# Kernel optimization log

Measured on AMD Instinct MI355X. Metric: run time of the kernel, lower is better.

Reference implementation:

```python
import jax, jax.numpy as jnp
import numpy as np

WINDOW = 64
STRIDE = 4
IMG_H = 512
IMG_W = 512


def _extract_windows(img, W, stride):
    # img: [H, Wd] -> windows [oh*ow, W, W] (row-major over the output grid,
    # matching torch F.unfold ordering)
    H, Wd = img.shape
    oh = (H - W) // stride + 1
    ow = (Wd - W) // stride + 1
    rows = (jnp.arange(oh) * stride)[:, None] + jnp.arange(W)[None, :]   # [oh, W]
    cols = (jnp.arange(ow) * stride)[:, None] + jnp.arange(W)[None, :]   # [ow, W]
    windows = img[rows[:, None, :, None], cols[None, :, None, :]]        # [oh, ow, W, W]
    return windows.reshape(oh * ow, W, W), oh, ow


def setup_inputs() -> dict:
    key = jax.random.key(0)
    X = jax.random.uniform(key, (1, 1, IMG_H, IMG_W), dtype=jnp.float32)
    return {"X": X}


def reference(X):
    W = WINDOW
    stride = STRIDE
    img = X[0, 0]
    windows, oh, ow = _extract_windows(img, W, stride)  # [N, W, W]

    # sizes = 2**arange(log2(W), 1, -1): e.g. W=64 -> [64, 32, 16, 8, 4]
    sizes = (2 ** np.arange(int(np.log2(W)), 1, -1)).astype(np.int64)
    log_sizes = jnp.log(jnp.asarray(sizes, dtype=jnp.float32))  # [S]

    log_db = []
    for s in sizes:
        s = int(s)
        # box partition of each window: [N, W//s, s, W//s, s]
        r = windows.reshape(-1, W // s, s, W // s, s)
        smax = r.max(axis=(2, 4))
        smin = r.min(axis=(2, 4))
        d_b = (smax - smin).sum(axis=(1, 2))  # [N] per-window box-count sum
        log_db.append(jnp.log(d_b))
    log_db = jnp.stack(log_db)  # [S, N]

    # lstsq with a single column (no intercept): slope = <x, y> / <x, x>
    slope = (log_sizes @ log_db) / (log_sizes @ log_sizes)  # [N]
    fd = -slope
    return fd.reshape(1, 1, oh, ow)
```

## Files before the change

### kernel.cpp

```cpp
#include <hip/hip_runtime.h>
#include <math.h>

#define IMG_W 512
#define OW 113
#define DS 27

__device__ __forceinline__ float max4f(float4 v) { return fmaxf(fmaxf(v.x, v.y), fmaxf(v.z, v.w)); }
__device__ __forceinline__ float min4f(float4 v) { return fminf(fminf(v.x, v.y), fminf(v.z, v.w)); }

__global__ __launch_bounds__(256) void fd_fused(const float* __restrict__ X,
                                                float* __restrict__ out) {
    const int bi = blockIdx.x / 15;
    const int bj = blockIdx.x - bi * 15;
    const int t  = threadIdx.x;

    __shared__ float tmax[23][24], tmin[23][24];
    __shared__ float p8x[22][24],  p8n[22][24];
    __shared__ float p16x[20][24], p16n[20][24];
    __shared__ float p32x[16][24], p32n[16][24];
    __shared__ float df4[23][DS], df8[22][DS], df16[20][DS], df32[16][DS];

    for (int idx = t; idx < 23 * 23; idx += 256) {
        const int lr = idx / 23, lc = idx - lr * 23;
        const int gr = min(bi * 8 + lr, 127);
        const int gc = min(bj * 8 + lc, 127);
        const float* p = X + (gr * 4) * IMG_W + gc * 4;
        float4 a = *(const float4*)(p);
        float4 b = *(const float4*)(p + IMG_W);
        float4 c = *(const float4*)(p + 2 * IMG_W);
        float4 d = *(const float4*)(p + 3 * IMG_W);
        float mx = fmaxf(fmaxf(max4f(a), max4f(b)), fmaxf(max4f(c), max4f(d)));
        float mn = fminf(fminf(min4f(a), min4f(b)), fminf(min4f(c), min4f(d)));
        tmax[lr][lc] = mx;
        tmin[lr][lc] = mn;
        df4[lr][lc]  = mx - mn;
    }
    __syncthreads();

    for (int idx = t; idx < 22 * 22; idx += 256) {
        const int lr = idx / 22, lc = idx - lr * 22;
        float x = fmaxf(fmaxf(tmax[lr][lc],     tmax[lr][lc + 1]),
                        fmaxf(tmax[lr + 1][lc], tmax[lr + 1][lc + 1]));
        float n = fminf(fminf(tmin[lr][lc],     tmin[lr][lc + 1]),
                        fminf(tmin[lr + 1][lc], tmin[lr + 1][lc + 1]));
        p8x[lr][lc] = x;
        p8n[lr][lc] = n;
        df8[lr][lc] = x - n;
    }
    __syncthreads();

    for (int idx = t; idx < 20 * 20; idx += 256) {
        const int lr = idx / 20, lc = idx - lr * 20;
        float x = fmaxf(fmaxf(p8x[lr][lc],     p8x[lr][lc + 2]),
                        fmaxf(p8x[lr + 2][lc], p8x[lr + 2][lc + 2]));
        float n = fminf(fminf(p8n[lr][lc],     p8n[lr][lc + 2]),
                        fminf(p8n[lr + 2][lc], p8n[lr + 2][lc + 2]));
        p16x[lr][lc] = x;
        p16n[lr][lc] = n;
        df16[lr][lc] = x - n;
    }
    __syncthreads();

    {
        const int lr = t >> 4, lc = t & 15;
        float x = fmaxf(fmaxf(p16x[lr][lc],     p16x[lr][lc + 4]),
                        fmaxf(p16x[lr + 4][lc], p16x[lr + 4][lc + 4]));
        float n = fminf(fminf(p16n[lr][lc],     p16n[lr][lc + 4]),
                        fminf(p16n[lr + 4][lc], p16n[lr + 4][lc + 4]));
        p32x[lr][lc] = x;
        p32n[lr][lc] = n;
        df32[lr][lc] = x - n;
    }
    __syncthreads();

    const int q  = t >> 2;
    const int pp = t & 3;
    const int wi = q >> 3, wj = q & 7;

    float d4 = 0.f;
    #pragma unroll
    for (int r = 0; r < 4; ++r) {
        const float* row = &df4[wi + 4 * pp + r][wj];
        #pragma unroll
        for (int b = 0; b < 16; ++b) d4 += row[b];
    }
    float d8 = 0.f;
    #pragma unroll
    for (int r = 0; r < 2; ++r) {
        const float* row = &df8[wi + 2 * (2 * pp + r)][wj];
        #pragma unroll
        for (int b = 0; b < 8; ++b) d8 += row[2 * b];
    }
    float d16 = 0.f;
    {
        const float* row = &df16[wi + 4 * pp][wj];
        #pragma unroll
        for (int b = 0; b < 4; ++b) d16 += row[4 * b];
    }
    float d32 = df32[wi + 8 * (pp >> 1)][wj + 8 * (pp & 1)];
    float d64 = 0.f;
    if (pp == 0) {
        float x = fmaxf(fmaxf(p32x[wi][wj],     p32x[wi][wj + 8]),
                        fmaxf(p32x[wi + 8][wj], p32x[wi + 8][wj + 8]));
        float n = fminf(fminf(p32n[wi][wj],     p32n[wi][wj + 8]),
                        fminf(p32n[wi + 8][wj], p32n[wi + 8][wj + 8]));
        d64 = x - n;
    }

    d4  += __shfl_down(d4,  2, 64);  d4  += __shfl_down(d4,  1, 64);
    d8  += __shfl_down(d8,  2, 64);  d8  += __shfl_down(d8,  1, 64);
    d16 += __shfl_down(d16, 2, 64);  d16 += __shfl_down(d16, 1, 64);
    d32 += __shfl_down(d32, 2, 64);  d32 += __shfl_down(d32, 1, 64);

    if (pp == 0) {
        const int gwi = bi * 8 + wi;
        const int gwj = bj * 8 + wj;
        if (gwi < OW && gwj < OW) {
            const float LN2 = 0.69314718055994530942f;
            const float num = 6.f * logf(d64) + 5.f * logf(d32) + 4.f * logf(d16)
                            + 3.f * logf(d8)  + 2.f * logf(d4);
            out[gwi * OW + gwj] = -num / (90.0f * LN2);
        }
    }
}

extern "C" void kernel_launch(void* const* d_in, const int* in_sizes, int n_in,
                              void* d_out, int out_size, void* d_ws, size_t ws_size,
                              hipStream_t stream) {
    const float* X = (const float*)d_in[0];
    float* out = (float*)d_out;
    fd_fused<<<15 * 15, 256, 0, stream>>>(X, out);
}
```

Baseline: 58.49 us.

## Precompute horizontal partial sums per level and pack max/min as float2

Adds a horizontal-sum stage per level (h4, h8, h16) that runs alongside the next pyramid level's computation. The final per-window reduction then reads a few partial sums instead of scanning up to 64 shared-memory entries per thread. Max/min pairs are stored interleaved as float2, so each neighbour fetch is one wider LDS access. The cost is extra shared-memory arrays, more work between barriers, and a possible change in bank-conflict patterns. It targets a kernel that is small and likely bound by launch overhead and latency.

```diff
diff --git a/kernel.cpp b/kernel.cpp
--- a/kernel.cpp
+++ b/kernel.cpp
@@ -3,7 +3,6 @@
 
 #define IMG_W 512
 #define OW 113
-#define DS 27
 
 __device__ __forceinline__ float max4f(float4 v) { return fmaxf(fmaxf(v.x, v.y), fmaxf(v.z, v.w)); }
 __device__ __forceinline__ float min4f(float4 v) { return fminf(fminf(v.x, v.y), fminf(v.z, v.w)); }
@@ -14,11 +13,12 @@
     const int bj = blockIdx.x - bi * 15;
     const int t  = threadIdx.x;
 
-    __shared__ float tmax[23][24], tmin[23][24];
-    __shared__ float p8x[22][24],  p8n[22][24];
-    __shared__ float p16x[20][24], p16n[20][24];
-    __shared__ float p32x[16][24], p32n[16][24];
-    __shared__ float df4[23][DS], df8[22][DS], df16[20][DS], df32[16][DS];
+    __shared__ float2 tmm[23][24];
+    __shared__ float2 p8[22][24];
+    __shared__ float2 p16[20][24];
+    __shared__ float2 p32[16][24];
+    __shared__ float df4[23][25], df8[22][25], df16[20][25], df32[16][25];
+    __shared__ float h4[23][9], h8[22][9], h16[20][9];
 
     for (int idx = t; idx < 23 * 23; idx += 256) {
         const int lr = idx / 23, lc = idx - lr * 23;
@@ -31,45 +31,62 @@
         float4 d = *(const float4*)(p + 3 * IMG_W);
         float mx = fmaxf(fmaxf(max4f(a), max4f(b)), fmaxf(max4f(c), max4f(d)));
         float mn = fminf(fminf(min4f(a), min4f(b)), fminf(min4f(c), min4f(d)));
-        tmax[lr][lc] = mx;
-        tmin[lr][lc] = mn;
-        df4[lr][lc]  = mx - mn;
+        tmm[lr][lc] = make_float2(mx, mn);
+        df4[lr][lc] = mx - mn;
     }
     __syncthreads();
 
     for (int idx = t; idx < 22 * 22; idx += 256) {
         const int lr = idx / 22, lc = idx - lr * 22;
-        float x = fmaxf(fmaxf(tmax[lr][lc],     tmax[lr][lc + 1]),
-                        fmaxf(tmax[lr + 1][lc], tmax[lr + 1][lc + 1]));
-        float n = fminf(fminf(tmin[lr][lc],     tmin[lr][lc + 1]),
-                        fminf(tmin[lr + 1][lc], tmin[lr + 1][lc + 1]));
-        p8x[lr][lc] = x;
-        p8n[lr][lc] = n;
+        float2 q00 = tmm[lr][lc],     q01 = tmm[lr][lc + 1];
+        float2 q10 = tmm[lr + 1][lc], q11 = tmm[lr + 1][lc + 1];
+        float x = fmaxf(fmaxf(q00.x, q01.x), fmaxf(q10.x, q11.x));
+        float n = fminf(fminf(q00.y, q01.y), fminf(q10.y, q11.y));
+        p8[lr][lc] = make_float2(x, n);
         df8[lr][lc] = x - n;
+    }
+    if (t < 23 * 8) {
+        const int r = t >> 3, wj = t & 7;
+        float s = 0.f;
+        #pragma unroll
+        for (int b = 0; b < 16; ++b) s += df4[r][wj + b];
+        h4[r][wj] = s;
     }
     __syncthreads();
 
     for (int idx = t; idx < 20 * 20; idx += 256) {
         const int lr = idx / 20, lc = idx - lr * 20;
-        float x = fmaxf(fmaxf(p8x[lr][lc],     p8x[lr][lc + 2]),
-                        fmaxf(p8x[lr + 2][lc], p8x[lr + 2][lc + 2]));
-        float n = fminf(fminf(p8n[lr][lc],     p8n[lr][lc + 2]),
-                        fminf(p8n[lr + 2][lc], p8n[lr + 2][lc + 2]));
-        p16x[lr][lc] = x;
-        p16n[lr][lc] = n;
+        float2 q00 = p8[lr][lc],     q01 = p8[lr][lc + 2];
+        float2 q10 = p8[lr + 2][lc], q11 = p8[lr + 2][lc + 2];
+        float x = fmaxf(fmaxf(q00.x, q01.x), fmaxf(q10.x, q11.x));
+        float n = fminf(fminf(q00.y, q01.y), fminf(q10.y, q11.y));
+        p16[lr][lc] = make_float2(x, n);
         df16[lr][lc] = x - n;
+    }
+    if (t < 22 * 8) {
+        const int r = t >> 3, wj = t & 7;
+        float s = 0.f;
+        #pragma unroll
+        for (int b = 0; b < 8; ++b) s += df8[r][wj + 2 * b];
+        h8[r][wj] = s;
     }
     __syncthreads();
 
     {
         const int lr = t >> 4, lc = t & 15;
-        float x = fmaxf(fmaxf(p16x[lr][lc],     p16x[lr][lc + 4]),
-                        fmaxf(p16x[lr + 4][lc], p16x[lr + 4][lc + 4]));
-        float n = fminf(fminf(p16n[lr][lc],     p16n[lr][lc + 4]),
-                        fminf(p16n[lr + 4][lc], p16n[lr + 4][lc + 4]));
-        p32x[lr][lc] = x;
-        p32n[lr][lc] = n;
+        float2 q00 = p16[lr][lc],     q01 = p16[lr][lc + 4];
+        float2 q10 = p16[lr + 4][lc], q11 = p16[lr + 4][lc + 4];
+        float x = fmaxf(fmaxf(q00.x, q01.x), fmaxf(q10.x, q11.x));
+        float n = fminf(fminf(q00.y, q01.y), fminf(q10.y, q11.y));
+        p32[lr][lc] = make_float2(x, n);
         df32[lr][lc] = x - n;
+    }
+    if (t < 20 * 8) {
+        const int r = t >> 3, wj = t & 7;
+        float s = 0.f;
+        #pragma unroll
+        for (int b = 0; b < 4; ++b) s += df16[r][wj + 4 * b];
+        h16[r][wj] = s;
     }
     __syncthreads();
 
@@ -77,40 +94,23 @@
     const int pp = t & 3;
     const int wi = q >> 3, wj = q & 7;
 
-    float d4 = 0.f;
-    #pragma unroll
-    for (int r = 0; r < 4; ++r) {
-        const float* row = &df4[wi + 4 * pp + r][wj];
-        #pragma unroll
-        for (int b = 0; b < 16; ++b) d4 += row[b];
-    }
-    float d8 = 0.f;
-    #pragma unroll
-    for (int r = 0; r < 2; ++r) {
-        const float* row = &df8[wi + 2 * (2 * pp + r)][wj];
-        #pragma unroll
-        for (int b = 0; b < 8; ++b) d8 += row[2 * b];
-    }
-    float d16 = 0.f;
-    {
-        const float* row = &df16[wi + 4 * pp][wj];
-        #pragma unroll
-        for (int b = 0; b < 4; ++b) d16 += row[4 * b];
-    }
-    float d32 = df32[wi + 8 * (pp >> 1)][wj + 8 * (pp & 1)];
-    float d64 = 0.f;
+    float d4 = h4[wi + 4 * pp][wj]     + h4[wi + 4 * pp + 1][wj]
+             + h4[wi + 4 * pp + 2][wj] + h4[wi + 4 * pp + 3][wj];
+    float d8 = h8[wi + 4 * pp][wj] + h8[wi + 4 * pp + 2][wj];
+    float d16 = h16[wi + 4 * pp][wj];
+    float d32 = 0.f, d64 = 0.f;
+    if (pp < 2) d32 = df32[wi + 8 * pp][wj] + df32[wi + 8 * pp][wj + 8];
     if (pp == 0) {
-        float x = fmaxf(fmaxf(p32x[wi][wj],     p32x[wi][wj + 8]),
-                        fmaxf(p32x[wi + 8][wj], p32x[wi + 8][wj + 8]));
-        float n = fminf(fminf(p32n[wi][wj],     p32n[wi][wj + 8]),
-                        fminf(p32n[wi + 8][wj], p32n[wi + 8][wj + 8]));
-        d64 = x - n;
+        float2 a0 = p32[wi][wj],     a1 = p32[wi][wj + 8];
+        float2 a2 = p32[wi + 8][wj], a3 = p32[wi + 8][wj + 8];
+        d64 = fmaxf(fmaxf(a0.x, a1.x), fmaxf(a2.x, a3.x))
+            - fminf(fminf(a0.y, a1.y), fminf(a2.y, a3.y));
     }
 
     d4  += __shfl_down(d4,  2, 64);  d4  += __shfl_down(d4,  1, 64);
     d8  += __shfl_down(d8,  2, 64);  d8  += __shfl_down(d8,  1, 64);
     d16 += __shfl_down(d16, 2, 64);  d16 += __shfl_down(d16, 1, 64);
-    d32 += __shfl_down(d32, 2, 64);  d32 += __shfl_down(d32, 1, 64);
+    d32 += __shfl_down(d32, 1, 64);
 
     if (pp == 0) {
         const int gwi = bi * 8 + wi;
```

New measurement: 57.12 us. -2.3%, faster.
